# Optimization experiments

Measured on AMD Instinct MI355X. Metric: run time of the kernel, lower is better.

Reference implementation:

```python
import jax, jax.numpy as jnp
import numpy as np
from jax import lax

K = 3      # kernel_size
C = 64     # n_feat
B, H, W = 2, 256, 256


def _conv(x, w, b, pad):
    # NCHW conv, stride 1
    out = lax.conv_general_dilated(x, w, (1, 1), [(pad, pad), (pad, pad)],
                                   dimension_numbers=('NCHW', 'OIHW', 'NCHW'))
    return out + b[None, :, None, None]


def _prelu(x, a):
    # nn.PReLU() with a single shared learnable slope (init 0.25)
    return jnp.where(x >= 0, x, a * x)


def setup_inputs():
    key = jax.random.key(0)
    ks = jax.random.split(key, 20)
    s = 0.05
    def w(k, shape):
        return jax.random.normal(k, shape, jnp.float32) * s
    inp = {
        'image': jax.random.normal(ks[0], (B, C, H, W), jnp.float32),
        'guidance': jax.random.normal(ks[1], (B, C, H, W), jnp.float32),
        # self.tensor: 1x1 conv (2C -> C) + PReLU (shared with jbf_conv's act)
        'tensor_w': w(ks[2], (C, 2 * C, 1, 1)),
        'tensor_b': jnp.zeros((C,), jnp.float32),
        'a_jbf': jnp.full((1,), 0.25, jnp.float32),
        'kg_w1': w(ks[3], (C, C, 3, 3)), 'kg_b1': jnp.zeros((C,), jnp.float32),
        'kg_w2': w(ks[4], (C, C, 3, 3)), 'kg_b2': jnp.zeros((C,), jnp.float32),
        'kg_w3': w(ks[5], (C, C, 3, 3)), 'kg_b3': jnp.zeros((C,), jnp.float32),
        'kg_w4': w(ks[6], (C, C, 3, 3)), 'kg_b4': jnp.zeros((C,), jnp.float32),
        'kg_w5': w(ks[7], (K * K * C, C, 1, 1)),
        'kg_b5': jnp.zeros((K * K * C,), jnp.float32),
        'a_kg': jnp.full((1,), 0.25, jnp.float32),
        # jbf_conv: 3x3 C->C, PReLU (shared a_jbf), 3x3 C->C
        'jbf_w1': w(ks[8], (C, C, 3, 3)), 'jbf_b1': jnp.zeros((C,), jnp.float32),
        'jbf_w2': w(ks[9], (C, C, 3, 3)), 'jbf_b2': jnp.zeros((C,), jnp.float32),
    }
    return inp


def reference(image, guidance, tensor_w, tensor_b, a_jbf,
              kg_w1, kg_b1, kg_w2, kg_b2, kg_w3, kg_b3, kg_w4, kg_b4,
              kg_w5, kg_b5, a_kg, jbf_w1, jbf_b1, jbf_w2, jbf_b2):
    b, c, h, w = image.shape
    # fuse target+guidance features
    t = _prelu(_conv(jnp.concatenate([image, guidance], axis=1), tensor_w, tensor_b, 0), a_jbf)
    # concat_kg: predict per-pixel dynamic kernel (b, K*K*c, h, w)
    y = t
    for wt, bs in ((kg_w1, kg_b1), (kg_w2, kg_b2), (kg_w3, kg_b3), (kg_w4, kg_b4)):
        y = _prelu(_conv(y, wt, bs, 1), a_kg)
    bi_kernel = _conv(y, kg_w5, kg_b5, 0)
    # unfold: torch layout is channel-major (c, ki, kj) along dim 1
    p = (K - 1) // 2
    xp = jnp.pad(image, ((0, 0), (0, 0), (p, p), (p, p)))
    taps = [xp[:, :, i:i + h, j:j + w] for i in range(K) for j in range(K)]
    patch = jnp.stack(taps, axis=2).reshape(b, c * K * K, h, w)
    # NOTE: faithful to source -- (c*K*K) flat layout reinterpreted as (K*K, c)
    jbf = (patch * bi_kernel).reshape(b, K * K, c, h, w).sum(axis=1)
    out = _conv(_prelu(_conv(jbf, jbf_w1, jbf_b1, 1), a_jbf), jbf_w2, jbf_b2, 1)
    return out + image
```

## Files before the change

kernel.cpp:

```cpp
#include <hip/hip_runtime.h>

#define HW 65536

typedef __bf16 bf16x8 __attribute__((ext_vector_type(8)));
typedef float f32x16 __attribute__((ext_vector_type(16)));

__device__ inline unsigned short f2bf(float x) {
    union { float f; unsigned u; } v; v.f = x;
    unsigned r = v.u + 0x7FFF + ((v.u >> 16) & 1);
    return (unsigned short)(r >> 16);
}
__device__ inline unsigned pk2(float a, float b) {
    unsigned r;
    asm("v_cvt_pk_bf16_f32 %0, %1, %2" : "=v"(r) : "v"(a), "v"(b));
    return r;
}
__device__ inline float bfhi2f(unsigned u) {
    union { unsigned u; float f; } v; v.u = u & 0xffff0000u; return v.f;
}
__device__ inline float bflo2f(unsigned u) {
    union { unsigned u; float f; } v; v.u = u << 16; return v.f;
}

union FragU { uint4 u; bf16x8 v; };
__device__ inline bf16x8 ld_frag(const uint4* p) { FragU t; t.u = *p; return t.v; }


__global__ __launch_bounds__(256) void k_pre(
    const float* __restrict__ img, const float* __restrict__ gd,
    const float* __restrict__ w0, const float* __restrict__ w1,
    const float* __restrict__ w2, const float* __restrict__ w3,
    const float* __restrict__ w4, const float* __restrict__ w5,
    const float* __restrict__ w5c, const float* __restrict__ tw,
    unsigned short* __restrict__ imgT, unsigned short* __restrict__ gdT,
    unsigned short* __restrict__ wT)
{
    __shared__ float sT[64 * 66];
    int tid = threadIdx.x;
    int y = blockIdx.y;
    if (y < 4) {
        int z = y;
        int b = z & 1;
        const float* src = (z >> 1) ? gd : img;
        unsigned short* dst = (z >> 1) ? gdT : imgT;
        int px0 = blockIdx.x * 64;
        size_t sbase = (size_t)b * 64 * HW + px0;

#pragma unroll
        for (int i = 0; i < 4; ++i) {
            int e = i * 256 + tid;
            int ic = e >> 4, seg = e & 15;
            float4 v = *(const float4*)(src + sbase + (size_t)ic * HW + seg * 4);
            float* p = &sT[ic * 66 + seg * 4];
            ((float2*)p)[0] = make_float2(v.x, v.y);
            ((float2*)p)[1] = make_float2(v.z, v.w);
        }
        __syncthreads();

        size_t dbase = (size_t)b * HW * 64 + (size_t)px0 * 64;
#pragma unroll
        for (int k = 0; k < 2; ++k) {
            int idx = k * 256 + tid;
            int px = idx >> 3, u = idx & 7;
            union { uint4 q; unsigned w[4]; } ou;
#pragma unroll
            for (int j = 0; j < 4; ++j)
                ou.w[j] = pk2(sT[(u * 8 + 2 * j) * 66 + px],
                              sT[(u * 8 + 2 * j + 1) * 66 + px]);
            *(uint4*)(dst + dbase + (size_t)px * 64 + u * 8) = ou.q;
        }
    } else {
        int y2 = y - 4;
        unsigned short* o = wT + (size_t)y2 * 36864;
        int e = blockIdx.x * 256 + tid;
        if (y2 < 6) {
            const float* ws_[6] = {w0, w1, w2, w3, w4, w5};
            const float* w = ws_[y2];
            if (e < 36864) {
                int tap = e >> 12, oc = (e >> 6) & 63, ic = e & 63;
                int igg = ic >> 3, j = ic & 7;
                int dst = ((tap * 8 + igg) * 64 + oc) * 8 + j;
                o[dst] = f2bf(w[(oc * 64 + ic) * 9 + tap]);
            }
        } else if (y2 == 6) {
            if (e < 36864) o[e] = f2bf(w5c[e]);
        } else {
            if (e < 8192) {
                int oc = e >> 7, ic = e & 127;
                int kg = ic >> 3, j = ic & 7;
                o[((kg * 64 + oc) << 3) + j] = f2bf(tw[e]);
            }
        }
    }
}

__global__ __launch_bounds__(256, 2) void k_fuse3(
    const unsigned short* __restrict__ imgT, const unsigned short* __restrict__ gdT,
    const unsigned short* __restrict__ wTf,
    const unsigned short* __restrict__ w1T, const unsigned short* __restrict__ w2T,
    const float* __restrict__ tb, const float* __restrict__ b1,
    const float* __restrict__ b2, const float* __restrict__ ajbf,
    const float* __restrict__ akg, unsigned short* __restrict__ out)
{
    __shared__ __align__(16) char smem[54528];
    float* sB = (float*)(smem + 53760);
    uint4* sS0 = (uint4*)smem;
    uint4* sS1 = (uint4*)(smem + 19200);

    int tid = threadIdx.x;
    int wv = tid >> 6, lane = tid & 63;
    int half = lane >> 5, l31 = lane & 31;
    int w2 = wv >> 1, g = wv & 1;
    int lin = blockIdx.x + (blockIdx.y << 4) + (blockIdx.z << 9);
    int slab = lin & 7, sub = lin >> 3;
    int b = slab >> 2;
    int y0 = (slab & 3) * 64 + (sub >> 4) * 8;
    int x0 = (sub & 15) * 16;
    const size_t zbase = (size_t)b * HW * 64;
    const uint4* wgf = (const uint4*)wTf;
    const uint4* wg1 = (const uint4*)w1T;
    const uint4* wg2 = (const uint4*)w2T;

    if (tid < 64) sB[tid] = tb[tid];
    else if (tid < 128) sB[tid] = b1[tid - 64];
    else if (tid < 192) sB[tid] = b2[tid - 128];

    auto loadS = [&](int t, int h, uint4* rx) {
        const unsigned short* src = t ? gdT : imgT;
#pragma unroll
        for (int i = 0; i < 4; ++i) {
            int e = i * 256 + tid;
            int cell = e >> 2, ig = e & 3;
            int r = cell / 20, c2 = cell - r * 20;
            int gy = y0 - 2 + r, gx = x0 - 2 + c2;
            rx[i] = make_uint4(0, 0, 0, 0);
            if (e < 960 && gy >= 0 && gy < 256 && gx >= 0 && gx < 256)
                rx[i] = *(const uint4*)(src + zbase + ((size_t)(gy * 256 + gx)) * 64 + h * 32 + ig * 8);
        }
    };
    auto writeS = [&](uint4* s, const uint4* rx) {
#pragma unroll
        for (int i = 0; i < 4; ++i) {
            int e = i * 256 + tid;
            if (e < 960) s[(e >> 2) * 5 + (e & 3)] = rx[i];
        }
    };

    int cell0[4];
#pragma unroll
    for (int s = 0; s < 4; ++s) {
        int c = g * 128 + s * 32 + l31;
        cell0[s] = c < 240 ? c : 239;
    }
    f32x16 acc0[4];
#pragma unroll
    for (int s = 0; s < 4; ++s)
#pragma unroll
        for (int r = 0; r < 16; ++r) acc0[s][r] = 0.f;

    auto mm1 = [&](int t, int h, const uint4* sS) {
        __builtin_amdgcn_s_setprio(1);
#pragma unroll
        for (int c = 0; c < 2; ++c) {
            int ig = c * 2 + half;
            int kg = t * 8 + h * 4 + ig;
            bf16x8 af = ld_frag(&wgf[kg * 64 + w2 * 32 + l31]);
#pragma unroll
            for (int s = 0; s < 4; ++s) {
                bf16x8 bb = ld_frag(&sS[cell0[s] * 5 + ig]);
                acc0[s] = __builtin_amdgcn_mfma_f32_32x32x16_bf16(af, bb, acc0[s], 0, 0, 0);
            }
        }
        __builtin_amdgcn_s_setprio(0);
    };

    uint4 rx[4];
    loadS(0, 0, rx);
    writeS(sS0, rx);
    loadS(0, 1, rx);
    __syncthreads();
    mm1(0, 0, sS0);
    writeS(sS1, rx);
    loadS(1, 0, rx);
    __syncthreads();
    mm1(0, 1, sS1);
    writeS(sS0, rx);
    loadS(1, 1, rx);
    __syncthreads();
    mm1(1, 0, sS0);
    writeS(sS1, rx);
    __syncthreads();
    mm1(1, 1, sS1);

    float s_jbf = ajbf[0], s_kg = akg[0];
    __syncthreads();
    unsigned short* sC0 = (unsigned short*)smem;
#pragma unroll
    for (int s = 0; s < 4; ++s) {
        int cell = g * 128 + s * 32 + l31;
        if (cell < 240) {
            int R = cell / 20, C = cell - R * 20;
            int gy = y0 - 2 + R, gx = x0 - 2 + C;
            bool inb = (gy >= 0 && gy < 256 && gx >= 0 && gx < 256);
#pragma unroll
            for (int q2 = 0; q2 < 4; ++q2) {
                float vv[4];
#pragma unroll
                for (int j = 0; j < 4; ++j) {
                    int r = (q2 << 2) | j;
                    int oc = w2 * 32 + j + 8 * q2 + 4 * half;
                    float v = acc0[s][r] + sB[oc];
                    v = (v >= 0.f) ? v : s_jbf * v;
                    vv[j] = inb ? v : 0.f;
                }
                int up = (w2 * 4 + q2) ^ (cell & 7);
                *(uint2*)&sC0[cell * 64 + up * 8 + half * 4] =
                    make_uint2(pk2(vv[0], vv[1]), pk2(vv[2], vv[3]));
            }
        }
    }
    __syncthreads();

    int cellv[3], ibv[3];
#pragma unroll
    for (int s = 0; s < 3; ++s) {
        int c = g * 96 + s * 32 + l31;
        cellv[s] = c;
        int cc = c < 180 ? c : 179;
        ibv[s] = (cc / 18) * 20 + (cc % 18);
    }
    f32x16 acc1[3];
#pragma unroll
    for (int s = 0; s < 3; ++s)
#pragma unroll
        for (int r = 0; r < 16; ++r) acc1[s][r] = 0.f;

    {
        const uint4* sC04 = (const uint4*)smem;
        __builtin_amdgcn_s_setprio(1);
#pragma unroll
        for (int dy = 0; dy < 3; ++dy) {
#pragma unroll
            for (int dx = 0; dx < 3; ++dx) {
                int tap = dy * 3 + dx;
                int doff = dy * 20 + dx;
#pragma unroll
                for (int c4 = 0; c4 < 4; ++c4) {
                    int unit = c4 * 2 + half;
                    bf16x8 af = ld_frag(&wg1[(tap * 8 + unit) * 64 + w2 * 32 + l31]);
#pragma unroll
                    for (int s = 0; s < 3; ++s) {
                        int cc = ibv[s] + doff;
                        bf16x8 bb = ld_frag(&sC04[cc * 8 + (unit ^ (cc & 7))]);
                        acc1[s] = __builtin_amdgcn_mfma_f32_32x32x16_bf16(af, bb, acc1[s], 0, 0, 0);
                    }
                }
            }
        }
        __builtin_amdgcn_s_setprio(0);
    }

    unsigned short* sC1 = (unsigned short*)(smem + 30720);
#pragma unroll
    for (int s = 0; s < 3; ++s) {
        int cell = cellv[s];
        if (cell < 180) {
            int orow = cell / 18, ocol = cell - orow * 18;
            int gy = y0 - 1 + orow, gx = x0 - 1 + ocol;
            bool inb = (gy >= 0 && gy < 256 && gx >= 0 && gx < 256);
#pragma unroll
            for (int q2 = 0; q2 < 4; ++q2) {
                float vv[4];
#pragma unroll
                for (int j = 0; j < 4; ++j) {
                    int r = (q2 << 2) | j;
                    int oc = w2 * 32 + j + 8 * q2 + 4 * half;
                    float v = acc1[s][r] + sB[64 + oc];
                    v = (v >= 0.f) ? v : s_kg * v;
                    vv[j] = inb ? v : 0.f;
                }
                int up = (w2 * 4 + q2) ^ (cell & 7);
                *(uint2*)&sC1[cell * 64 + up * 8 + half * 4] =
                    make_uint2(pk2(vv[0], vv[1]), pk2(vv[2], vv[3]));
            }
        }
    }
    __syncthreads();

    f32x16 acc2[2];
#pragma unroll
    for (int s = 0; s < 2; ++s)
#pragma unroll
        for (int r = 0; r < 16; ++r) acc2[s][r] = 0.f;

    int rowS[2], colS[2];
#pragma unroll
    for (int s = 0; s < 2; ++s) {
        int px = g * 64 + s * 32 + l31;
        rowS[s] = px >> 4; colS[s] = px & 15;
    }
    {
        const uint4* sC14 = (const uint4*)(smem + 30720);
        __builtin_amdgcn_s_setprio(1);
#pragma unroll
        for (int dy = 0; dy < 3; ++dy) {
#pragma unroll
            for (int dx = 0; dx < 3; ++dx) {
                int tap = dy * 3 + dx;
#pragma unroll
                for (int c = 0; c < 4; ++c) {
                    int ig = c * 2 + half;
                    bf16x8 af = ld_frag(&wg2[(tap * 8 + ig) * 64 + w2 * 32 + l31]);
#pragma unroll
                    for (int s = 0; s < 2; ++s) {
                        int cl = (rowS[s] + dy) * 18 + colS[s] + dx;
                        bf16x8 bb = ld_frag(&sC14[cl * 8 + (ig ^ (cl & 7))]);
                        acc2[s] = __builtin_amdgcn_mfma_f32_32x32x16_bf16(af, bb, acc2[s], 0, 0, 0);
                    }
                }
            }
        }
        __builtin_amdgcn_s_setprio(0);
    }

    unsigned short* sT16 = (unsigned short*)smem;
#pragma unroll
    for (int s = 0; s < 2; ++s) {
        int px = g * 64 + s * 32 + l31;
#pragma unroll
        for (int q2 = 0; q2 < 4; ++q2) {
            float vv[4];
#pragma unroll
            for (int j = 0; j < 4; ++j) {
                int r = (q2 << 2) | j;
                int oc = w2 * 32 + j + 8 * q2 + 4 * half;
                float v = acc2[s][r] + sB[128 + oc];
                vv[j] = (v >= 0.f) ? v : s_kg * v;
            }
            int up = (w2 * 4 + q2) ^ (px & 7);
            uint2* p = (uint2*)&sT16[px * 64 + up * 8 + half * 4];
            *p = make_uint2(pk2(vv[0], vv[1]), pk2(vv[2], vv[3]));
        }
    }
    __syncthreads();
#pragma unroll
    for (int k = 0; k < 4; ++k) {
        int idx = k * 256 + tid;
        int row = idx >> 7, rem = idx & 127;
        int col = rem >> 3, u = rem & 7;
        int px = row * 16 + col;
        uint4 v = *(uint4*)&sT16[px * 64 + (u ^ (px & 7)) * 8];
        *(uint4*)(out + zbase + ((size_t)((y0 + row) * 256 + x0 + col)) * 64 + u * 8) = v;
    }
}

#define XU 5

template<int MODE>
__global__ __launch_bounds__(256, 4) void k_conv2x(
    const unsigned short* __restrict__ in,
    const unsigned short* __restrict__ w1T, const unsigned short* __restrict__ w2T,
    const float* __restrict__ b1, const float* __restrict__ b2,
    const float* __restrict__ a, const float* __restrict__ res,
    void* __restrict__ outv)
{
    __shared__ __align__(16) char smem[38912];
    uint4* sIn0 = (uint4*)smem;
    uint4* sIn1 = (uint4*)(smem + 19200);
    float* sB = (float*)(smem + 38400);

    int tid = threadIdx.x;
    int wv = tid >> 6, lane = tid & 63;
    int half = lane >> 5, l31 = lane & 31;
    int w2 = wv >> 1, g = wv & 1;
    int lin = blockIdx.x + (blockIdx.y << 4) + (blockIdx.z << 9);
    int slab = lin & 7, sub = lin >> 3;
    int b = slab >> 2;
    int y0 = (slab & 3) * 64 + (sub >> 4) * 8;
    int x0 = (sub & 15) * 16;
    const size_t zbase = (size_t)b * HW * 64;
    const uint4* wg1 = (const uint4*)w1T;
    const uint4* wg2 = (const uint4*)w2T;

    if (tid < 64) sB[tid] = b1[tid];
    else if (tid < 128) sB[tid] = b2[tid - 64];

    auto loadIn = [&](int h, uint4* rx) {
#pragma unroll
        for (int i = 0; i < 4; ++i) {
            int e = i * 256 + tid;
            int cell = e >> 2, ig = e & 3;
            int r = cell / 20, c2 = cell - r * 20;
            int gy = y0 - 2 + r, gx = x0 - 2 + c2;
            rx[i] = make_uint4(0, 0, 0, 0);
            bool act = (i < 3) || (e < 960);
            if (act && gy >= 0 && gy < 256 && gx >= 0 && gx < 256)
                rx[i] = *(const uint4*)(in + zbase + ((size_t)(gy * 256 + gx)) * 64 + h * 32 + ig * 8);
        }
    };
    auto writeIn = [&](uint4* s, const uint4* rx) {
#pragma unroll
        for (int i = 0; i < 4; ++i) {
            int e = i * 256 + tid;
            if (i < 3 || e < 960) s[(e >> 2) * XU + (e & 3)] = rx[i];
        }
    };

    int cellv[3], ibv[3];
#pragma unroll
    for (int s = 0; s < 3; ++s) {
        int c = g * 96 + s * 32 + l31;
        cellv[s] = c;
        int cc = c < 180 ? c : 179;
        ibv[s] = (cc / 18) * 20 + (cc % 18);
    }

    f32x16 acc1[3];
#pragma unroll
    for (int s = 0; s < 3; ++s)
#pragma unroll
        for (int r = 0; r < 16; ++r) acc1[s][r] = 0.f;

    auto conv1_h = [&](int h, const uint4* sInp) {
        __builtin_amdgcn_s_setprio(1);
#pragma unroll
        for (int dy = 0; dy < 3; ++dy) {
#pragma unroll
            for (int dx = 0; dx < 3; ++dx) {
                int tap = dy * 3 + dx;
                int doff = dy * 20 + dx;
#pragma unroll
                for (int c = 0; c < 2; ++c) {
                    int ig = c * 2 + half;
                    bf16x8 af = ld_frag(&wg1[(tap * 8 + h * 4 + ig) * 64 + w2 * 32 + l31]);
#pragma unroll
                    for (int s = 0; s < 3; ++s) {
                        bf16x8 bb = ld_frag(&sInp[(ibv[s] + doff) * XU + ig]);
                        acc1[s] = __builtin_amdgcn_mfma_f32_32x32x16_bf16(af, bb, acc1[s], 0, 0, 0);
                    }
                }
            }
        }
        __builtin_amdgcn_s_setprio(0);
    };

    uint4 rx[4];
    loadIn(0, rx);
    writeIn(sIn0, rx);
    uint4 ry[4];
    loadIn(1, ry);
    __syncthreads();
    conv1_h(0, sIn0);
    writeIn(sIn1, ry);
    __syncthreads();
    conv1_h(1, sIn1);

    float s1 = a[0];
    __syncthreads();
    unsigned short* sC16 = (unsigned short*)smem;
#pragma unroll
    for (int s = 0; s < 3; ++s) {
        int cell = cellv[s];
        if (cell < 180) {
            int orow = cell / 18, ocol = cell - orow * 18;
            int gy = y0 - 1 + orow, gx = x0 - 1 + ocol;
            bool inb = (gy >= 0 && gy < 256 && gx >= 0 && gx < 256);
#pragma unroll
            for (int q2 = 0; q2 < 4; ++q2) {
                float vv[4];
#pragma unroll
                for (int j = 0; j < 4; ++j) {
                    int r = (q2 << 2) | j;
                    int oc = w2 * 32 + j + 8 * q2 + 4 * half;
                    float v = acc1[s][r] + sB[oc];
                    v = (v >= 0.f) ? v : s1 * v;
                    vv[j] = inb ? v : 0.f;
                }
                int up = (w2 * 4 + q2) ^ (cell & 7);
                *(uint2*)&sC16[cell * 64 + up * 8 + half * 4] =
                    make_uint2(pk2(vv[0], vv[1]), pk2(vv[2], vv[3]));
            }
        }
    }
    __syncthreads();

    f32x16 acc2[2];
#pragma unroll
    for (int s = 0; s < 2; ++s)
#pragma unroll
        for (int r = 0; r < 16; ++r) acc2[s][r] = 0.f;

    int rowS[2], colS[2];
#pragma unroll
    for (int s = 0; s < 2; ++s) {
        int px = g * 64 + s * 32 + l31;
        rowS[s] = px >> 4; colS[s] = px & 15;
    }
    {
        const uint4* sC4 = (const uint4*)smem;
        __builtin_amdgcn_s_setprio(1);
#pragma unroll
        for (int dy = 0; dy < 3; ++dy) {
#pragma unroll
            for (int dx = 0; dx < 3; ++dx) {
                int tap = dy * 3 + dx;
#pragma unroll
                for (int c = 0; c < 4; ++c) {
                    int ig = c * 2 + half;
                    bf16x8 af = ld_frag(&wg2[(tap * 8 + ig) * 64 + w2 * 32 + l31]);
#pragma unroll
                    for (int s = 0; s < 2; ++s) {
                        int cl = (rowS[s] + dy) * 18 + colS[s] + dx;
                        bf16x8 bb = ld_frag(&sC4[cl * 8 + (ig ^ (cl & 7))]);
                        acc2[s] = __builtin_amdgcn_mfma_f32_32x32x16_bf16(af, bb, acc2[s], 0, 0, 0);
                    }
                }
            }
        }
        __builtin_amdgcn_s_setprio(0);
    }

    if (MODE == 0) {
        __syncthreads();
        unsigned short* sT16 = (unsigned short*)smem;
#pragma unroll
        for (int s = 0; s < 2; ++s) {
            int px = g * 64 + s * 32 + l31;
#pragma unroll
            for (int q2 = 0; q2 < 4; ++q2) {
                float vv[4];
#pragma unroll
                for (int j = 0; j < 4; ++j) {
                    int r = (q2 << 2) | j;
                    int oc = w2 * 32 + j + 8 * q2 + 4 * half;
                    float v = acc2[s][r] + sB[64 + oc];
                    vv[j] = (v >= 0.f) ? v : s1 * v;
                }
                int up = (w2 * 4 + q2) ^ (px & 7);
                uint2* p = (uint2*)&sT16[px * 64 + up * 8 + half * 4];
                *p = make_uint2(pk2(vv[0], vv[1]), pk2(vv[2], vv[3]));
            }
        }
        __syncthreads();
        unsigned short* outT = (unsigned short*)outv;
#pragma unroll
        for (int k = 0; k < 4; ++k) {
            int idx = k * 256 + tid;
            int row = idx >> 7, rem = idx & 127;
            int col = rem >> 3, u = rem & 7;
            int px = row * 16 + col;
            uint4 v = *(uint4*)&sT16[px * 64 + (u ^ (px & 7)) * 8];
            *(uint4*)(outT + zbase + ((size_t)((y0 + row) * 256 + x0 + col)) * 64 + u * 8) = v;
        }
    } else {
        float* outF = (float*)outv;
#pragma unroll
        for (int s = 0; s < 2; ++s) {
            int px = g * 64 + s * 32 + l31;
            int y = y0 + (px >> 4), x = x0 + (px & 15);
            size_t pbase = (size_t)b * 64 * HW + (size_t)y * 256 + x;
#pragma unroll
            for (int r = 0; r < 16; ++r) {
                int oc = w2 * 32 + (r & 3) + 8 * (r >> 2) + 4 * half;
                float v = acc2[s][r] + sB[64 + oc];
                v += res[pbase + (size_t)oc * HW];
                outF[pbase + (size_t)oc * HW] = v;
            }
        }
    }
}

struct OffTab { unsigned v[9][32]; int chlo[9]; };
constexpr OffTab make_tab() {
    OffTab t{};
    for (int kk = 0; kk < 9; ++kk) {
        int chlo = (kk * 64) / 9;
        t.chlo[kk] = chlo;
        for (int ot = 0; ot < 2; ++ot)
            for (int r = 0; r < 16; ++r) {
                int cc0 = ot * 32 + (r & 3) + 8 * (r >> 2);
                int q0 = kk * 64 + cc0, q1 = q0 + 4;
                int o0 = (q0 / 9 - chlo) * 360 + (q0 % 9 / 3) * 40 + (q0 % 9 % 3);
                int o1 = (q1 / 9 - chlo) * 360 + (q1 % 9 / 3) * 40 + (q1 % 9 % 3);
                t.v[kk][ot * 16 + r] = (unsigned)o0 | ((unsigned)o1 << 16);
            }
    }
    return t;
}
__constant__ OffTab kOff = make_tab();

__global__ __launch_bounds__(256, 2) void k_jbfm5(
    const unsigned short* __restrict__ in, const float* __restrict__ img,
    const unsigned short* __restrict__ w1T, const unsigned short* __restrict__ w2T,
    const unsigned short* __restrict__ w5T,
    const float* __restrict__ b1, const float* __restrict__ b2,
    const float* __restrict__ b5, const float* __restrict__ akg,
    unsigned short* __restrict__ out)
{
    __shared__ __align__(16) char smem[80896];
    float* sB = (float*)(smem + 80384);
    uint4* sIn0 = (uint4*)smem;
    uint4* sIn1 = (uint4*)(smem + 34560);
    uint4* sY = (uint4*)(smem + 43520);
    float* sB5 = (float*)(smem + 39424);
    unsigned short* sT16 = (unsigned short*)smem;

    int tid = threadIdx.x;
    int wv = tid >> 6, lane = tid & 63;
    int half = lane >> 5, l31 = lane & 31;
    int w2 = wv >> 1, g = wv & 1;
    int lin = blockIdx.x + (blockIdx.y << 3) + (blockIdx.z << 8);
    int slab = lin & 7, sub = lin >> 3;
    int b = slab >> 2;
    int y0 = (slab & 3) * 64 + (sub >> 3) * 8;
    int x0 = (sub & 7) * 32;
    size_t zbase = (size_t)b * HW * 64;
    size_t ibase = (size_t)b * 64 * HW;
    const uint4* wg1 = (const uint4*)w1T;
    const uint4* wg2 = (const uint4*)w2T;

    if (tid < 64) sB[tid] = b1[tid];
    else if (tid < 128) sB[tid] = b2[tid - 64];

    auto loadIn = [&](int h, uint4* rx) {
#pragma unroll
        for (int i = 0; i < 7; ++i) {
            int e = i * 256 + tid;
            int cell = e >> 2, ig = e & 3;
            int r = cell / 36, c2 = cell - r * 36;
            int gy = y0 - 2 + r, gx = x0 - 2 + c2;
            rx[i] = make_uint4(0, 0, 0, 0);
            if (e < 1728 && gy >= 0 && gy < 256 && gx >= 0 && gx < 256)
                rx[i] = *(const uint4*)(in + zbase + ((size_t)(gy * 256 + gx)) * 64 + h * 32 + ig * 8);
        }
    };
    auto writeIn = [&](uint4* s, const uint4* rx) {
#pragma unroll
        for (int i = 0; i < 7; ++i) {
            int e = i * 256 + tid;
            if (e < 1728) s[(e >> 2) * XU + (e & 3)] = rx[i];
        }
    };

    int cellv[6], ibv[6];
    bool val[6];
#pragma unroll
    for (int s = 0; s < 6; ++s) {
        int c = g * 170 + s * 32 + l31;
        val[s] = (s * 32 + l31) < 170;
        cellv[s] = c;
        int cc = c < 340 ? c : 339;
        ibv[s] = (cc / 34) * 36 + (cc % 34);
    }
    f32x16 acc1[6];
#pragma unroll
    for (int s = 0; s < 6; ++s)
#pragma unroll
        for (int r = 0; r < 16; ++r) acc1[s][r] = 0.f;

    auto conv1_h = [&](int h, const uint4* sInp) {
        __builtin_amdgcn_s_setprio(1);
#pragma unroll
        for (int dy = 0; dy < 3; ++dy) {
#pragma unroll
            for (int dx = 0; dx < 3; ++dx) {
                int tap = dy * 3 + dx;
                int doff = dy * 36 + dx;
#pragma unroll
                for (int c = 0; c < 2; ++c) {
                    int ig = c * 2 + half;
                    bf16x8 af = ld_frag(&wg1[(tap * 8 + h * 4 + ig) * 64 + w2 * 32 + l31]);
#pragma unroll
                    for (int s = 0; s < 6; ++s) {
                        bf16x8 bb = ld_frag(&sInp[(ibv[s] + doff) * XU + ig]);
                        acc1[s] = __builtin_amdgcn_mfma_f32_32x32x16_bf16(af, bb, acc1[s], 0, 0, 0);
                    }
                }
            }
        }
        __builtin_amdgcn_s_setprio(0);
    };

    uint4 rx[7], ry[7];
    loadIn(0, rx);
    writeIn(sIn0, rx);
    loadIn(1, ry);
    __syncthreads();
    conv1_h(0, sIn0);
    writeIn(sIn1, ry);
    __syncthreads();
    conv1_h(1, sIn1);

    float s_kg = akg[0];
    __syncthreads();
    unsigned short* sC16 = (unsigned short*)smem;
#pragma unroll
    for (int s = 0; s < 6; ++s) {
        if (val[s]) {
            int cell = cellv[s];
            int row = cell / 34, col = cell - row * 34;
            int gy = y0 - 1 + row, gx = x0 - 1 + col;
            bool inb = (gy >= 0 && gy < 256 && gx >= 0 && gx < 256);
#pragma unroll
            for (int q2 = 0; q2 < 4; ++q2) {
                float vv[4];
#pragma unroll
                for (int j = 0; j < 4; ++j) {
                    int r = (q2 << 2) | j;
                    int oc = w2 * 32 + j + 8 * q2 + 4 * half;
                    float v = acc1[s][r] + sB[oc];
                    v = (v >= 0.f) ? v : s_kg * v;
                    vv[j] = inb ? v : 0.f;
                }
                int up = (w2 * 4 + q2) ^ (cell & 7);
                *(uint2*)&sC16[cell * 64 + up * 8 + half * 4] =
                    make_uint2(pk2(vv[0], vv[1]), pk2(vv[2], vv[3]));
            }
        }
    }
    __syncthreads();

    f32x16 acc2[4];
#pragma unroll
    for (int s = 0; s < 4; ++s)
#pragma unroll
        for (int r = 0; r < 16; ++r) acc2[s][r] = 0.f;

    int rowS[4], colS[4];
#pragma unroll
    for (int s = 0; s < 4; ++s) {
        int p = g * 128 + s * 32 + l31;
        rowS[s] = p >> 5; colS[s] = p & 31;
    }
    {
        const uint4* sC4 = (const uint4*)smem;
        __builtin_amdgcn_s_setprio(1);
#pragma unroll
        for (int dy = 0; dy < 3; ++dy) {
#pragma unroll
            for (int dx = 0; dx < 3; ++dx) {
                int tap = dy * 3 + dx;
#pragma unroll
                for (int c = 0; c < 4; ++c) {
                    int ig = c * 2 + half;
                    bf16x8 af = ld_frag(&wg2[(tap * 8 + ig) * 64 + w2 * 32 + l31]);
#pragma unroll
                    for (int s = 0; s < 4; ++s) {
                        int cl = (rowS[s] + dy) * 34 + colS[s] + dx;
                        bf16x8 bb = ld_frag(&sC4[cl * 8 + (ig ^ (cl & 7))]);
                        acc2[s] = __builtin_amdgcn_mfma_f32_32x32x16_bf16(af, bb, acc2[s], 0, 0, 0);
                    }
                }
            }
        }
        __builtin_amdgcn_s_setprio(0);
    }

    {
        unsigned short* sY16 = (unsigned short*)(smem + 43520);
#pragma unroll
        for (int s = 0; s < 4; ++s) {
            int px = g * 128 + s * 32 + l31;
#pragma unroll
            for (int q2 = 0; q2 < 4; ++q2) {
                int ig = w2 * 4 + q2;
                float vv[4];
#pragma unroll
                for (int j = 0; j < 4; ++j) {
                    int r = (q2 << 2) | j;
                    int oc = w2 * 32 + j + 8 * q2 + 4 * half;
                    float v = acc2[s][r] + sB[64 + oc];
                    vv[j] = (v >= 0.f) ? v : s_kg * v;
                }
                *(uint2*)&sY16[px * 72 + ig * 8 + half * 4] =
                    make_uint2(pk2(vv[0], vv[1]), pk2(vv[2], vv[3]));
            }
        }
    }
    __syncthreads();

    int p_off[3], p_dst[3];
    bool p_a[3], p_b[3], p_act[3];
#pragma unroll
    for (int i = 0; i < 3; ++i) {
        int e = i * 256 + tid;
        bool act = e < 720;
        int ch = e / 90, rem = e - ch * 90;
        int rp = rem / 10, seg = rem - rp * 10;
        int gy = y0 + rp - 1;
        int gxb = x0 - 4 + seg * 4;
        bool xok = (gxb >= 0 && gxb < 256);
        p_act[i] = act;
        p_a[i] = act && xok && gy >= 0 && gy < 256;
        p_b[i] = act && xok && (gy + 1) < 256;
        p_off[i] = ch * HW + gy * 256 + gxb;
        p_dst[i] = ch * 360 + rp * 40 + seg * 4;
    }

    for (int e = tid; e < 576; e += 256) sB5[e] = b5[e];

    {
        uint4* sW50 = (uint4*)smem;
        unsigned* sP0 = (unsigned*)(smem + 16384);
#pragma unroll
        for (int u = 0; u < 2; ++u) {
            int uu = u * 256 + tid;
            int cc = uu & 63, ig = uu >> 6;
            sW50[uu] = ((const uint4*)w5T)[cc * 8 + ig];
        }
        const float* rp0 = img + ibase;
#pragma unroll
        for (int i = 0; i < 3; ++i) {
            float4 fa = make_float4(0, 0, 0, 0), fb = make_float4(0, 0, 0, 0);
            if (p_a[i]) fa = *(const float4*)(rp0 + p_off[i]);
            if (p_b[i]) fb = *(const float4*)(rp0 + p_off[i] + 256);
            if (p_act[i]) {
                uint4 pk;
                pk.x = pk2(fa.x, fb.x);
                pk.y = pk2(fa.y, fb.y);
                pk.z = pk2(fa.z, fb.z);
                pk.w = pk2(fa.w, fb.w);
                *(uint4*)&sP0[p_dst[i]] = pk;
            }
        }
    }

    float jb[2][2][16];
#pragma unroll
    for (int i = 0; i < 2; ++i)
#pragma unroll
        for (int j = 0; j < 2; ++j)
#pragma unroll
            for (int r = 0; r < 16; ++r) jb[i][j][r] = 0.f;

    __syncthreads();

#pragma unroll 1
    for (int kk = 0; kk < 9; ++kk) {
        const int cur = kk & 1;
        const uint4* sW5c = (const uint4*)(smem + cur * 8192);
        const unsigned* sPc = (const unsigned*)(smem + 16384 + cur * 11520);

        uint4 wpre0, wpre1;
        float4 pfa[3], pfb[3];
        if (kk < 8) {
            const int nk = kk + 1;
            const int chlo_n = kOff.chlo[nk];
            {
                int cc = tid & 63, ig = tid >> 6;
                wpre0 = ((const uint4*)w5T)[(nk * 64 + cc) * 8 + ig];
                int uu = 256 + tid;
                int cc1 = uu & 63, ig1 = uu >> 6;
                wpre1 = ((const uint4*)w5T)[(nk * 64 + cc1) * 8 + ig1];
            }
            const float* rp0 = img + ibase + (size_t)chlo_n * HW;
#pragma unroll
            for (int i = 0; i < 3; ++i) {
                pfa[i] = make_float4(0, 0, 0, 0);
                pfb[i] = make_float4(0, 0, 0, 0);
                if (p_a[i]) pfa[i] = *(const float4*)(rp0 + p_off[i]);
                if (p_b[i]) pfb[i] = *(const float4*)(rp0 + p_off[i] + 256);
            }
        }

        f32x16 acc[2][2];
#pragma unroll
        for (int ot = 0; ot < 2; ++ot)
#pragma unroll
            for (int r = 0; r < 16; ++r) {
                int cc0 = ot * 32 + (r & 3) + 8 * (r >> 2);
                float bv = sB5[kk * 64 + cc0 + 4 * half];
                acc[ot][0][r] = bv;
                acc[ot][1][r] = bv;
            }

        __builtin_amdgcn_s_setprio(1);
#pragma unroll
        for (int c = 0; c < 4; ++c) {
            int ig = c * 2 + half;
            bf16x8 a0 = ld_frag(&sW5c[ig * 64 + l31]);
            bf16x8 a1 = ld_frag(&sW5c[ig * 64 + 32 + l31]);
            int p0 = wv * 64 + l31;
            bf16x8 b0 = ld_frag(&sY[p0 * 9 + ig]);
            bf16x8 b1 = ld_frag(&sY[(p0 + 32) * 9 + ig]);
            acc[0][0] = __builtin_amdgcn_mfma_f32_32x32x16_bf16(a0, b0, acc[0][0], 0, 0, 0);
            acc[0][1] = __builtin_amdgcn_mfma_f32_32x32x16_bf16(a0, b1, acc[0][1], 0, 0, 0);
            acc[1][0] = __builtin_amdgcn_mfma_f32_32x32x16_bf16(a1, b0, acc[1][0], 0, 0, 0);
            acc[1][1] = __builtin_amdgcn_mfma_f32_32x32x16_bf16(a1, b1, acc[1][1], 0, 0, 0);
        }
        __builtin_amdgcn_s_setprio(0);

        {
            const unsigned* basep = sPc + wv * 80 + l31 + 3;
            const unsigned* tab = kOff.v[kk];
#pragma unroll
            for (int ot = 0; ot < 2; ++ot)
#pragma unroll
                for (int r = 0; r < 16; ++r) {
                    unsigned oo = tab[ot * 16 + r];
                    unsigned o0 = oo & 0xffffu, o1 = oo >> 16;
                    unsigned pv = basep[half ? o1 : o0];
                    jb[ot][0][r] = fmaf(acc[ot][0][r], bflo2f(pv), jb[ot][0][r]);
                    jb[ot][1][r] = fmaf(acc[ot][1][r], bfhi2f(pv), jb[ot][1][r]);
                }
        }

        if (kk < 8) {
            uint4* sW5n = (uint4*)(smem + (cur ^ 1) * 8192);
            unsigned* sPn = (unsigned*)(smem + 16384 + (cur ^ 1) * 11520);
            sW5n[tid] = wpre0;
            sW5n[256 + tid] = wpre1;
#pragma unroll
            for (int i = 0; i < 3; ++i) {
                if (p_act[i]) {
                    uint4 pk;
                    pk.x = pk2(pfa[i].x, pfb[i].x);
                    pk.y = pk2(pfa[i].y, pfb[i].y);
                    pk.z = pk2(pfa[i].z, pfb[i].z);
                    pk.w = pk2(pfa[i].w, pfb[i].w);
                    *(uint4*)&sPn[p_dst[i]] = pk;
                }
            }
        }
        __syncthreads();
    }

#pragma unroll
    for (int ot = 0; ot < 2; ++ot)
#pragma unroll
        for (int pt = 0; pt < 2; ++pt) {
            int px = wv * 64 + pt * 32 + l31;
#pragma unroll
            for (int q2 = 0; q2 < 4; ++q2) {
                int r0 = q2 << 2;
                int unit = ot * 4 + q2;
                int up = unit ^ (px & 7);
                uint2* p = (uint2*)&sT16[px * 64 + up * 8 + half * 4];
                *p = make_uint2(pk2(jb[ot][pt][r0], jb[ot][pt][r0 + 1]),
                                pk2(jb[ot][pt][r0 + 2], jb[ot][pt][r0 + 3]));
            }
        }
    __syncthreads();
#pragma unroll
    for (int k = 0; k < 8; ++k) {
        int col = tid >> 3, u = tid & 7;
        int px = k * 32 + col;
        uint4 v = *(uint4*)&sT16[px * 64 + (u ^ (px & 7)) * 8];
        *(uint4*)(out + zbase + ((size_t)((y0 + k) * 256 + x0 + col)) * 64 + u * 8) = v;
    }
}

extern "C" void kernel_launch(void* const* d_in, const int* in_sizes, int n_in,
                              void* d_out, int out_size, void* d_ws, size_t ws_size,
                              hipStream_t stream) {
    const float* img  = (const float*)d_in[0];
    const float* gd   = (const float*)d_in[1];
    const float* tw   = (const float*)d_in[2];
    const float* tb   = (const float*)d_in[3];
    const float* ajbf = (const float*)d_in[4];
    const float* kw1  = (const float*)d_in[5];
    const float* kb1  = (const float*)d_in[6];
    const float* kw2  = (const float*)d_in[7];
    const float* kb2  = (const float*)d_in[8];
    const float* kw3  = (const float*)d_in[9];
    const float* kb3  = (const float*)d_in[10];
    const float* kw4  = (const float*)d_in[11];
    const float* kb4  = (const float*)d_in[12];
    const float* kw5  = (const float*)d_in[13];
    const float* kb5  = (const float*)d_in[14];
    const float* akg  = (const float*)d_in[15];
    const float* jw1  = (const float*)d_in[16];
    const float* jb1  = (const float*)d_in[17];
    const float* jw2  = (const float*)d_in[18];
    const float* jb2  = (const float*)d_in[19];
    float* out  = (float*)d_out;

    const size_t TEN = (size_t)2 * HW * 64;
    unsigned short* bufA = (unsigned short*)d_ws;
    unsigned short* imgT = bufA + TEN;
    unsigned short* gdT  = imgT + TEN;
    unsigned short* wT   = gdT + TEN;
    unsigned short* bufC = gdT;

    dim3 gs(16, 32, 2);
    dim3 gw(8, 32, 2);

    k_pre<<<dim3(1024, 12), 256, 0, stream>>>(img, gd, kw1, kw2, kw3, kw4,
                                              jw1, jw2, kw5, tw, imgT, gdT, wT);

    k_fuse3<<<gs, 256, 0, stream>>>(imgT, gdT, wT + (size_t)7 * 36864,
                                    wT + (size_t)0 * 36864, wT + (size_t)1 * 36864,
                                    tb, kb1, kb2, ajbf, akg, bufA);

    k_jbfm5<<<gw, 256, 0, stream>>>(bufA, img,
                                    wT + (size_t)2 * 36864, wT + (size_t)3 * 36864,
                                    wT + (size_t)6 * 36864,
                                    kb3, kb4, kb5, akg, bufC);

    k_conv2x<2><<<gs, 256, 0, stream>>>(bufC, wT + (size_t)4 * 36864, wT + (size_t)5 * 36864,
                                        jb1, jb2, ajbf, img, out);
}
```

Measured before the change: 272.1 us.

## Flatten weight prep into one grid row, keep biases in registers, raise fuse3 occupancy

The weight-conversion work in k_pre moves from eight grid rows to a single row that covers all weight tensors with a grid-stride loop, so the grid shrinks from 12 to 5 rows. In k_fuse3 the bias values are held in per-thread registers instead of shared memory, which drops the bias LDS region and its loads. The launch-bounds occupancy hint rises from 2 to 3 blocks per SM. The extra 48 bias registers and the tighter register cap may force spills in this MFMA-heavy kernel.

```diff
diff --git a/kernel.cpp b/kernel.cpp
--- a/kernel.cpp
+++ b/kernel.cpp
@@ -70,31 +70,28 @@
             *(uint4*)(dst + dbase + (size_t)px * 64 + u * 8) = ou.q;
         }
     } else {
-        int y2 = y - 4;
-        unsigned short* o = wT + (size_t)y2 * 36864;
-        int e = blockIdx.x * 256 + tid;
-        if (y2 < 6) {
-            const float* ws_[6] = {w0, w1, w2, w3, w4, w5};
-            const float* w = ws_[y2];
-            if (e < 36864) {
-                int tap = e >> 12, oc = (e >> 6) & 63, ic = e & 63;
+        const float* ws_[6] = {w0, w1, w2, w3, w4, w5};
+        for (int e = blockIdx.x * 256 + tid; e < 266240; e += 262144) {
+            if (e < 221184) {
+                int y2 = e / 36864, e2 = e - y2 * 36864;
+                int tap = e2 >> 12, oc = (e2 >> 6) & 63, ic = e2 & 63;
                 int igg = ic >> 3, j = ic & 7;
                 int dst = ((tap * 8 + igg) * 64 + oc) * 8 + j;
-                o[dst] = f2bf(w[(oc * 64 + ic) * 9 + tap]);
-            }
-        } else if (y2 == 6) {
-            if (e < 36864) o[e] = f2bf(w5c[e]);
-        } else {
-            if (e < 8192) {
-                int oc = e >> 7, ic = e & 127;
+                wT[(size_t)y2 * 36864 + dst] = f2bf(ws_[y2][(oc * 64 + ic) * 9 + tap]);
+            } else if (e < 258048) {
+                int e2 = e - 221184;
+                wT[(size_t)6 * 36864 + e2] = f2bf(w5c[e2]);
+            } else {
+                int e2 = e - 258048;
+                int oc = e2 >> 7, ic = e2 & 127;
                 int kg = ic >> 3, j = ic & 7;
-                o[((kg * 64 + oc) << 3) + j] = f2bf(tw[e]);
+                wT[(size_t)7 * 36864 + ((kg * 64 + oc) << 3) + j] = f2bf(tw[e2]);
             }
         }
     }
 }
 
-__global__ __launch_bounds__(256, 2) void k_fuse3(
+__global__ __launch_bounds__(256, 3) void k_fuse3(
     const unsigned short* __restrict__ imgT, const unsigned short* __restrict__ gdT,
     const unsigned short* __restrict__ wTf,
     const unsigned short* __restrict__ w1T, const unsigned short* __restrict__ w2T,
@@ -102,8 +99,7 @@
     const float* __restrict__ b2, const float* __restrict__ ajbf,
     const float* __restrict__ akg, unsigned short* __restrict__ out)
 {
-    __shared__ __align__(16) char smem[54528];
-    float* sB = (float*)(smem + 53760);
+    __shared__ __align__(16) char smem[53760];
     uint4* sS0 = (uint4*)smem;
     uint4* sS1 = (uint4*)(smem + 19200);
 
@@ -121,9 +117,16 @@
     const uint4* wg1 = (const uint4*)w1T;
     const uint4* wg2 = (const uint4*)w2T;
 
-    if (tid < 64) sB[tid] = tb[tid];
-    else if (tid < 128) sB[tid] = b1[tid - 64];
-    else if (tid < 192) sB[tid] = b2[tid - 128];
+    float rT[16], rB1[16], rB2[16];
+#pragma unroll
+    for (int q2 = 0; q2 < 4; ++q2)
+#pragma unroll
+        for (int j = 0; j < 4; ++j) {
+            int oc = w2 * 32 + j + 8 * q2 + 4 * half;
+            rT[q2 * 4 + j]  = tb[oc];
+            rB1[q2 * 4 + j] = b1[oc];
+            rB2[q2 * 4 + j] = b2[oc];
+        }
 
     auto loadS = [&](int t, int h, uint4* rx) {
         const unsigned short* src = t ? gdT : imgT;
@@ -208,8 +211,7 @@
 #pragma unroll
                 for (int j = 0; j < 4; ++j) {
                     int r = (q2 << 2) | j;
-                    int oc = w2 * 32 + j + 8 * q2 + 4 * half;
-                    float v = acc0[s][r] + sB[oc];
+                    float v = acc0[s][r] + rT[q2 * 4 + j];
                     v = (v >= 0.f) ? v : s_jbf * v;
                     vv[j] = inb ? v : 0.f;
                 }
@@ -274,8 +276,7 @@
 #pragma unroll
                 for (int j = 0; j < 4; ++j) {
                     int r = (q2 << 2) | j;
-                    int oc = w2 * 32 + j + 8 * q2 + 4 * half;
-                    float v = acc1[s][r] + sB[64 + oc];
+                    float v = acc1[s][r] + rB1[q2 * 4 + j];
                     v = (v >= 0.f) ? v : s_kg * v;
                     vv[j] = inb ? v : 0.f;
                 }
@@ -333,8 +334,7 @@
 #pragma unroll
             for (int j = 0; j < 4; ++j) {
                 int r = (q2 << 2) | j;
-                int oc = w2 * 32 + j + 8 * q2 + 4 * half;
-                float v = acc2[s][r] + sB[128 + oc];
+                float v = acc2[s][r] + rB2[q2 * 4 + j];
                 vv[j] = (v >= 0.f) ? v : s_kg * v;
             }
             int up = (w2 * 4 + q2) ^ (px & 7);
@@ -985,8 +985,8 @@
     dim3 gs(16, 32, 2);
     dim3 gw(8, 32, 2);
 
-    k_pre<<<dim3(1024, 12), 256, 0, stream>>>(img, gd, kw1, kw2, kw3, kw4,
-                                              jw1, jw2, kw5, tw, imgT, gdT, wT);
+    k_pre<<<dim3(1024, 5), 256, 0, stream>>>(img, gd, kw1, kw2, kw3, kw4,
+                                             jw1, jw2, kw5, tw, imgT, gdT, wT);
 
     k_fuse3<<<gs, 256, 0, stream>>>(imgT, gdT, wT + (size_t)7 * 36864,
                                     wT + (size_t)0 * 36864, wT + (size_t)1 * 36864,
```

Result: no change. 273.1 us (+0.4%).
